# Kernel tuning notes

Hardware: AMD Instinct MI355X
Metric: run time of the kernel (lower is better)

The kernel has to match this reference:

```python
import jax, jax.numpy as jnp
import numpy as np

S_DIM = 128            # attention head width s
E_DIM = 1024           # expansion e = 2*hidden
SQRT_S = 128.0 ** 0.5
EPS = 1e-5


def setup_inputs() -> dict:
    key = jax.random.key(0)
    ks = jax.random.split(key, 8)
    B, S, H = 64, 512, 512
    uv_dim = 2 * E_DIM + S_DIM  # 2176
    # xavier-uniform-ish scale for uv weight
    lim = (6.0 / (H + uv_dim)) ** 0.5
    return {
        "x": jax.random.normal(ks[0], (B, S, H), dtype=jnp.float32),
        "ln_g": jnp.ones((1,), dtype=jnp.float32),
        "uv_w": jax.random.uniform(ks[1], (uv_dim, H), minval=-lim, maxval=lim, dtype=jnp.float32),
        "uv_b": jnp.zeros((uv_dim,), dtype=jnp.float32),
        "gamma": jax.random.uniform(ks[2], (2, S_DIM), dtype=jnp.float32),
        "beta": jax.random.uniform(ks[3], (2, S_DIM), dtype=jnp.float32),
        "w_bias": jax.random.uniform(ks[4], (2 * S - 1,), dtype=jnp.float32),
        "o_w": jax.random.normal(ks[5], (H, E_DIM), dtype=jnp.float32) * 0.02,
        "o_b": jnp.zeros((H,), dtype=jnp.float32),
    }


def _rope(x):
    # x: [B, S, 2, s]; rotate along the sequence dim (dim=1)
    S = x.shape[1]
    half = x.shape[-1] // 2
    pos = jnp.arange(S, dtype=jnp.float32)
    # torch: freq_seq = -arange(half)/half; inv_freq = 10000**(-freq_seq)
    inv_freq = 10000.0 ** (jnp.arange(half, dtype=jnp.float32) / half)
    sinus = pos[:, None, None] * inv_freq[None, None, :]  # [S, 1, half]
    sin, cos = jnp.sin(sinus), jnp.cos(sinus)
    x1, x2 = x[..., :half], x[..., half:]
    return jnp.concatenate([x1 * cos - x2 * sin, x2 * cos + x1 * sin], axis=-1)


def reference(x, ln_g, uv_w, uv_b, gamma, beta, w_bias, o_w, o_b):
    B, S, H = x.shape
    # ScaleNorm
    norm = jnp.linalg.norm(x, axis=-1, keepdims=True) * (H ** -0.5)
    xn = x / jnp.maximum(norm, EPS) * ln_g
    # fused uv projection + SiLU
    act = jax.nn.silu(xn @ uv_w.T + uv_b)  # [B, S, 2e+s]
    u = act[..., :E_DIM]
    v = act[..., E_DIM:2 * E_DIM]
    base = act[..., 2 * E_DIM:]                      # [B, S, s]
    base = base[:, :, None, :] * gamma + beta        # [B, S, 2, s]
    base = _rope(base)
    q, k = base[:, :, 0, :], base[:, :, 1, :]
    # scores + relative position bias: bias[i, j] = w[j - i + S - 1]
    qk = jnp.einsum('bsd,btd->bst', q, k)
    idx = jnp.arange(S)[None, :] - jnp.arange(S)[:, None] + (S - 1)
    qk = qk + w_bias[idx]
    # relu2 similarity kernel
    kernel = jnp.square(jax.nn.relu(qk / SQRT_S))    # [B, S, S]
    out = u * jnp.einsum('bst,bte->bse', kernel, v)  # gated attention
    out = out @ o_w.T + o_b
    return out + x  # use_shortcut: hidden == output
```

## Files before the change

### kernel.cpp

```cpp
#include <hip/hip_runtime.h>
#include <math.h>


#define M_TOT   32768
#define S_LEN   512
#define H_DIM   512
#define E_DIMC  1024
#define UV_DIM  2176
#define UV_PAD  2304
#define D_DIM   128

using floatx4  = __attribute__((ext_vector_type(4))) float;
using uintx2   = __attribute__((ext_vector_type(2))) unsigned int;
using uintx4   = __attribute__((ext_vector_type(4))) unsigned int;
using ushortx4 = __attribute__((ext_vector_type(4))) unsigned short;
using short8   = __attribute__((ext_vector_type(8))) short;

#define ASYNC_CP16(gsrc, ldst)                                                  \
    __builtin_amdgcn_global_load_lds(                                           \
        (const __attribute__((address_space(1))) void*)(gsrc),                  \
        (__attribute__((address_space(3))) void*)(ldst), 16, 0, 0)

__device__ __forceinline__ float bf2f(unsigned short h) {
    union { unsigned int u; float f; } c;
    c.u = ((unsigned int)h) << 16;
    return c.f;
}
__device__ __forceinline__ unsigned short f2bf(float f) {
    union { float f; unsigned int u; } c;
    c.f = f;
    unsigned int r = c.u + 0x7fffu + ((c.u >> 16) & 1u);
    return (unsigned short)(r >> 16);
}
__device__ __forceinline__ float silu_fast(float x) {
    float e = __expf(-x);
    return x * __builtin_amdgcn_rcpf(1.0f + e);
}
__device__ __forceinline__ int xcd_remap(int b, int nwg) {
    return (b & 7) * (nwg >> 3) + (b >> 3);
}

__global__ __launch_bounds__(256) void prep_kernel(const float* __restrict__ x,
                                                   const float* __restrict__ ln_g,
                                                   unsigned short* __restrict__ xn,
                                                   const float* __restrict__ uv_w,
                                                   unsigned short* __restrict__ uvwb,
                                                   const float* __restrict__ o_w,
                                                   unsigned short* __restrict__ owb,
                                                   float* __restrict__ cost,
                                                   float* __restrict__ sint) {
    const int bid = blockIdx.x;
    const int tid = threadIdx.x;
    if (bid < 8192) {
        int row  = bid * 4 + (tid >> 6);
        int lane = tid & 63;
        const float* xr = x + (size_t)row * H_DIM;
        floatx4 v0 = ((const floatx4*)xr)[lane];
        floatx4 v1 = ((const floatx4*)xr)[lane + 64];
        float ss = v0.x*v0.x + v0.y*v0.y + v0.z*v0.z + v0.w*v0.w
                 + v1.x*v1.x + v1.y*v1.y + v1.z*v1.z + v1.w*v1.w;
        #pragma unroll
        for (int off = 32; off > 0; off >>= 1) ss += __shfl_xor(ss, off, 64);
        float norm = sqrtf(ss) * 0.044194173824159216f;
        float sc   = ln_g[0] / fmaxf(norm, 1e-5f);
        unsigned short* xo = xn + (size_t)row * H_DIM;
        ushortx4 o0, o1;
        o0.x = f2bf(v0.x * sc); o0.y = f2bf(v0.y * sc);
        o0.z = f2bf(v0.z * sc); o0.w = f2bf(v0.w * sc);
        o1.x = f2bf(v1.x * sc); o1.y = f2bf(v1.y * sc);
        o1.z = f2bf(v1.z * sc); o1.w = f2bf(v1.w * sc);
        ((ushortx4*)xo)[lane]      = o0;
        ((ushortx4*)xo)[lane + 64] = o1;
    } else if (bid < 9344) {
        int i = (bid - 8192) * 256 + tid;
        ushortx4 o;
        if (i < UV_DIM * H_DIM / 4) {
            floatx4 v = ((const floatx4*)uv_w)[i];
            o.x = f2bf(v.x); o.y = f2bf(v.y); o.z = f2bf(v.z); o.w = f2bf(v.w);
        } else {
            o.x = 0; o.y = 0; o.z = 0; o.w = 0;
        }
        ((ushortx4*)uvwb)[i] = o;
    } else if (bid < 9856) {
        int i = (bid - 9344) * 256 + tid;
        floatx4 v = ((const floatx4*)o_w)[i];
        ushortx4 o;
        o.x = f2bf(v.x); o.y = f2bf(v.y); o.z = f2bf(v.z); o.w = f2bf(v.w);
        ((ushortx4*)owb)[i] = o;
    } else {
        int idx = (bid - 9856) * 256 + tid;
        int s = idx >> 6;
        int j = idx & 63;
        float invf = (float)pow(10000.0, (double)j / 64.0);
        float ang  = (float)s * invf;
        double a   = (double)ang;
        cost[s * 64 + j] = (float)cos(a);
        sint[s * 64 + j] = (float)sin(a);
    }
}

template <bool SWAPT>
__device__ __forceinline__ void gemm128_core(const unsigned short* __restrict__ A,
                                             const unsigned short* __restrict__ B,
                                             int lda, int ldb, int K,
                                             int m0, int n0,
                                             unsigned short (&st)[3][12288],
                                             floatx4 (&acc)[4][4]) {
    const int tid  = threadIdx.x;
    const int lane = tid & 63;
    const int wave = tid >> 6;
    const int quad = lane >> 4;
    const int l16  = lane & 15;
    const int wrow = (wave >> 2) * 64;
    const int wcol = (wave & 3) * 64;

    const int qa  = wave * 64 + lane;
    const int Ra  = qa >> 3;
    const int ca  = (qa & 7) ^ (Ra & 7);
    const int srA = 2 * Ra + (ca >> 2);
    const int scA = (ca & 3) * 8;
    const unsigned short* pa  = A + (size_t)(m0 + srA) * lda + scA;
    const unsigned short* pb0 = B + (size_t)(n0 + srA) * ldb + scA;
    const unsigned short* pb1 = pb0 + (size_t)128 * ldb;
    const int ldsA  = (wave * 64) * 8;
    const int ldsB0 = 4096 + (wave * 64) * 8;
    const int ldsB1 = 4096 + (512 + wave * 64) * 8;

    #pragma unroll
    for (int i = 0; i < 4; i++)
        #pragma unroll
        for (int j = 0; j < 4; j++) acc[i][j] = (floatx4){0.f, 0.f, 0.f, 0.f};

    const int NT = K >> 5;
    auto stage = [&](int buf, int t) {
        unsigned short* s = &st[buf][0];
        const int kt = t * 32;
        ASYNC_CP16(pa  + kt, s + ldsA);
        ASYNC_CP16(pb0 + kt, s + ldsB0);
        ASYNC_CP16(pb1 + kt, s + ldsB1);
    };
    stage(0, 0);
    stage(1, 1);

    int aoff[4], boff[4];
    #pragma unroll
    for (int mt = 0; mt < 4; mt++) {
        int r  = wrow + mt * 16 + l16;
        int Rr = r >> 1;
        int cp = (((r & 1) << 2) + quad) ^ (Rr & 7);
        aoff[mt] = Rr * 64 + cp * 8;
    }
    #pragma unroll
    for (int nt = 0; nt < 4; nt++) {
        int r  = wcol + nt * 16 + l16;
        int Rr = r >> 1;
        int cp = (((r & 1) << 2) + quad) ^ (Rr & 7);
        boff[nt] = 4096 + Rr * 64 + cp * 8;
    }

    int bc = 0, bs = 2;
    for (int t = 0; t < NT; ++t) {
        if (t < NT - 1) asm volatile("s_waitcnt vmcnt(3)" ::: "memory");
        else            asm volatile("s_waitcnt vmcnt(0)" ::: "memory");
        __builtin_amdgcn_sched_barrier(0);
        __builtin_amdgcn_s_barrier();
        __builtin_amdgcn_sched_barrier(0);
        if (t + 2 < NT) stage(bs, t + 2);

        const unsigned short* sb = &st[bc][0];
        short8 af[4], bf[4];
        #pragma unroll
        for (int mt = 0; mt < 4; mt++) {
            union { short8 s8; uintx4 u4; } fu;
            fu.u4 = *(const uintx4*)&sb[aoff[mt]];
            af[mt] = fu.s8;
        }
        #pragma unroll
        for (int nt = 0; nt < 4; nt++) {
            union { short8 s8; uintx4 u4; } fu;
            fu.u4 = *(const uintx4*)&sb[boff[nt]];
            bf[nt] = fu.s8;
        }
        __builtin_amdgcn_s_setprio(1);
        #pragma unroll
        for (int mt = 0; mt < 4; mt++)
            #pragma unroll
            for (int nt = 0; nt < 4; nt++)
                acc[mt][nt] = SWAPT
                    ? __builtin_amdgcn_mfma_f32_16x16x32_bf16(bf[nt], af[mt], acc[mt][nt], 0, 0, 0)
                    : __builtin_amdgcn_mfma_f32_16x16x32_bf16(af[mt], bf[nt], acc[mt][nt], 0, 0, 0);
        __builtin_amdgcn_s_setprio(0);

        bc = (bc == 2) ? 0 : bc + 1;
        bs = (bs == 2) ? 0 : bs + 1;
    }
}

union __align__(16) Lds3 {
    unsigned short st[3][12288];
    unsigned short T[128 * 256];
    float          Tf[128][132];
};

__global__ __launch_bounds__(512, 2) void gemm1_128_kernel(const unsigned short* __restrict__ xn,
                                                           const unsigned short* __restrict__ uvw,
                                                           const float* __restrict__ uvb,
                                                           unsigned short* __restrict__ u,
                                                           unsigned short* __restrict__ vT,
                                                           const float* __restrict__ gamma,
                                                           const float* __restrict__ beta,
                                                           const float* __restrict__ cost,
                                                           const float* __restrict__ sint,
                                                           unsigned short* __restrict__ q,
                                                           unsigned short* __restrict__ k) {
    __shared__ Lds3 lds;
    floatx4 acc[4][4];
    const int bl = blockIdx.y * 9 + blockIdx.x;
    const int lg = xcd_remap(bl, 9 * (M_TOT / 128));
    const int xb = lg % 9;
    const int m0 = (lg / 9) * 128;
    const int tid = threadIdx.x, lane = tid & 63, wave = tid >> 6;
    const int quad = lane >> 4, l16 = lane & 15;
    const int wrow = (wave >> 2) * 64, wcol = (wave & 3) * 64;

    if (xb < 4) {
        const int n0 = xb * 256;
        gemm128_core<true>(xn, uvw, H_DIM, H_DIM, H_DIM, m0, n0, lds.st, acc);
        __syncthreads();
        #pragma unroll
        for (int mt = 0; mt < 4; mt++) {
            int row = wrow + mt * 16 + l16;
            #pragma unroll
            for (int nt = 0; nt < 4; nt++) {
                int nl = wcol + nt * 16 + quad * 4;
                floatx4 b4 = *(const floatx4*)&uvb[n0 + nl];
                ushortx4 pk;
                #pragma unroll
                for (int r = 0; r < 4; r++)
                    pk[r] = f2bf(silu_fast(acc[mt][nt][r] + b4[r]));
                *(uintx2*)&lds.T[row * 256 + (((nl >> 3) ^ (row & 15)) << 3) + (nl & 7)] = *(uintx2*)&pk;
            }
        }
        __syncthreads();
        #pragma unroll
        for (int i = 0; i < 8; i++) {
            int idx = tid + i * 512;
            int row = idx >> 5, c16 = idx & 31;
            *(uintx4*)(u + (size_t)(m0 + row) * E_DIMC + n0 + c16 * 8) =
                *(const uintx4*)&lds.T[row * 256 + ((c16 ^ (row & 15)) << 3)];
        }
    } else if (xb < 8) {
        const int n0 = xb * 256;
        gemm128_core<false>(xn, uvw, H_DIM, H_DIM, H_DIM, m0, n0, lds.st, acc);
        __syncthreads();
        #pragma unroll
        for (int nt = 0; nt < 4; nt++) {
            int rowT = wcol + nt * 16 + l16;
            float bias = uvb[n0 + rowT];
            #pragma unroll
            for (int mt = 0; mt < 4; mt++) {
                int colT = wrow + mt * 16 + quad * 4;
                ushortx4 pk;
                #pragma unroll
                for (int r = 0; r < 4; r++)
                    pk[r] = f2bf(silu_fast(acc[mt][nt][r] + bias));
                *(uintx2*)&lds.T[rowT * 128 + (((colT >> 3) ^ (rowT & 15)) << 3) + (colT & 7)] = *(uintx2*)&pk;
            }
        }
        __syncthreads();
        const int b = m0 >> 9, sg0 = m0 & (S_LEN - 1), eg0 = n0 - E_DIMC;
        #pragma unroll
        for (int i = 0; i < 8; i++) {
            int idx = tid + i * 512;
            int e = idx >> 4, j = idx & 15;
            *(uintx4*)(vT + ((size_t)b * E_DIMC + eg0 + e) * S_LEN + sg0 + j * 8) =
                *(const uintx4*)&lds.T[e * 128 + ((j ^ (e & 15)) << 3)];
        }
    } else {
        const int n0 = 2048;
        gemm128_core<false>(xn, uvw, H_DIM, H_DIM, H_DIM, m0, n0, lds.st, acc);
        __syncthreads();
        if ((wave & 3) < 2) {
            #pragma unroll
            for (int mt = 0; mt < 4; mt++) {
                int rowl = wrow + mt * 16 + quad * 4;
                #pragma unroll
                for (int nt = 0; nt < 4; nt++) {
                    int n = wcol + nt * 16 + l16;
                    float bias = uvb[2048 + n];
                    #pragma unroll
                    for (int r = 0; r < 4; r++)
                        lds.Tf[rowl + r][n] = silu_fast(acc[mt][nt][r] + bias);
                }
            }
        }
        __syncthreads();
        #pragma unroll
        for (int i = 0; i < 16; i++) {
            int idx = tid + i * 512;
            int row = idx >> 6, j = idx & 63;
            int s   = (m0 + row) & (S_LEN - 1);
            float b1 = lds.Tf[row][j];
            float b2 = lds.Tf[row][j + 64];
            float c  = cost[s * 64 + j];
            float sn = sint[s * 64 + j];
            float yq1 = b1 * gamma[j]       + beta[j];
            float yq2 = b2 * gamma[64 + j]  + beta[64 + j];
            float yk1 = b1 * gamma[128 + j] + beta[128 + j];
            float yk2 = b2 * gamma[192 + j] + beta[192 + j];
            size_t mo = (size_t)(m0 + row) * D_DIM;
            q[mo + j]      = f2bf(yq1 * c - yq2 * sn);
            q[mo + 64 + j] = f2bf(yq2 * c + yq1 * sn);
            k[mo + j]      = f2bf(yk1 * c - yk2 * sn);
            k[mo + 64 + j] = f2bf(yk2 * c + yk1 * sn);
        }
    }
}

template <bool SWAPT>
__device__ __forceinline__ void gemm256_core(const unsigned short* __restrict__ A,
                                             const unsigned short* __restrict__ B,
                                             int lda, int ldb, int K,
                                             int m0, int n0,
                                             unsigned short (&st)[4][2][128][64],
                                             floatx4 (&acc)[8][4]) {
    const int tid  = threadIdx.x;
    const int lane = tid & 63;
    const int wave = tid >> 6;
    const int quad = lane >> 4;
    const int l16  = lane & 15;
    const int wrow = (wave >> 2) * 128;
    const int wcol = (wave & 3) * 64;

    const int q0    = wave * 128 + lane;
    const int R0    = q0 >> 3;
    const int cp0   = q0 & 7;
    const int c0    = cp0 ^ (R0 & 7);
    const int srow0 = 2 * R0 + (c0 >> 2);
    const int scol0 = (c0 & 3) * 8;

    const unsigned short* pa0 = A + (size_t)(m0 + srow0) * lda + scol0;
    const unsigned short* pa1 = pa0 + (size_t)16 * lda;
    const unsigned short* pb0 = B + (size_t)(n0 + srow0) * ldb + scol0;
    const unsigned short* pb1 = pb0 + (size_t)16 * ldb;
    const int ldsOff0 = (wave * 128) * 8;
    const int ldsOff1 = (wave * 128 + 64) * 8;

    #pragma unroll
    for (int i = 0; i < 8; i++)
        #pragma unroll
        for (int j = 0; j < 4; j++) acc[i][j] = (floatx4){0.f, 0.f, 0.f, 0.f};

    const int NT = K >> 5;
    auto stage = [&](int t) {
        unsigned short* sA = &st[t & 3][0][0][0];
        unsigned short* sB = &st[t & 3][1][0][0];
        const int kt = t * 32;
        ASYNC_CP16(pa0 + kt, sA + ldsOff0);
        ASYNC_CP16(pa1 + kt, sA + ldsOff1);
        ASYNC_CP16(pb0 + kt, sB + ldsOff0);
        ASYNC_CP16(pb1 + kt, sB + ldsOff1);
    };
    stage(0);
    stage(1);
    stage(2);

    int aoff[8], boff[4];
    #pragma unroll
    for (int mt = 0; mt < 8; mt++) {
        int r  = wrow + mt * 16 + l16;
        int Rr = r >> 1;
        int cp = (((r & 1) << 2) + quad) ^ (Rr & 7);
        aoff[mt] = Rr * 64 + cp * 8;
    }
    #pragma unroll
    for (int nt = 0; nt < 4; nt++) {
        int r  = wcol + nt * 16 + l16;
        int Rr = r >> 1;
        int cp = (((r & 1) << 2) + quad) ^ (Rr & 7);
        boff[nt] = Rr * 64 + cp * 8;
    }

    for (int t = 0; t < NT; ++t) {
        if (t < NT - 2)       asm volatile("s_waitcnt vmcnt(8)" ::: "memory");
        else if (t == NT - 2) asm volatile("s_waitcnt vmcnt(4)" ::: "memory");
        else                  asm volatile("s_waitcnt vmcnt(0)" ::: "memory");
        __builtin_amdgcn_sched_barrier(0);
        __builtin_amdgcn_s_barrier();
        __builtin_amdgcn_sched_barrier(0);
        if (t + 3 < NT) stage(t + 3);

        const unsigned short* sA = &st[t & 3][0][0][0];
        const unsigned short* sB = &st[t & 3][1][0][0];
        short8 bf[4];
        #pragma unroll
        for (int nt = 0; nt < 4; nt++) {
            union { short8 s8; uintx4 u4; } fu;
            fu.u4 = *(const uintx4*)&sB[boff[nt]];
            bf[nt] = fu.s8;
        }
        #pragma unroll
        for (int half = 0; half < 2; half++) {
            short8 af[4];
            #pragma unroll
            for (int mt = 0; mt < 4; mt++) {
                union { short8 s8; uintx4 u4; } fu;
                fu.u4 = *(const uintx4*)&sA[aoff[half * 4 + mt]];
                af[mt] = fu.s8;
            }
            __builtin_amdgcn_s_setprio(1);
            #pragma unroll
            for (int mt = 0; mt < 4; mt++)
                #pragma unroll
                for (int nt = 0; nt < 4; nt++)
                    acc[half * 4 + mt][nt] = SWAPT
                        ? __builtin_amdgcn_mfma_f32_16x16x32_bf16(bf[nt], af[mt], acc[half * 4 + mt][nt], 0, 0, 0)
                        : __builtin_amdgcn_mfma_f32_16x16x32_bf16(af[mt], bf[nt], acc[half * 4 + mt][nt], 0, 0, 0);
            __builtin_amdgcn_s_setprio(0);
        }
    }
}

__global__ __launch_bounds__(512, 2) void gemm_out256_kernel(const unsigned short* __restrict__ oe,
                                                             const unsigned short* __restrict__ ow,
                                                             const float* __restrict__ ob,
                                                             const float* __restrict__ x,
                                                             float* __restrict__ out) {
    __shared__ __align__(16) unsigned short st[4][2][128][64];
    floatx4 acc[8][4];
    const int bl = blockIdx.y * 2 + blockIdx.x;
    const int lg = xcd_remap(bl, 2 * (M_TOT / 256));
    const int n0 = (lg & 1) * 256;
    const int m0 = (lg >> 1) * 256;
    gemm256_core<true>(oe, ow, E_DIMC, E_DIMC, E_DIMC, m0, n0, st, acc);

    const int tid = threadIdx.x, lane = tid & 63, wave = tid >> 6;
    const int quad = lane >> 4, l16 = lane & 15;
    const int wrow = (wave >> 2) * 128, wcol = (wave & 3) * 64;
    #pragma unroll
    for (int mt = 0; mt < 8; mt++) {
        int m = m0 + wrow + mt * 16 + l16;
        #pragma unroll
        for (int nt = 0; nt < 4; nt++) {
            int n = n0 + wcol + nt * 16 + quad * 4;
            size_t off = (size_t)m * H_DIM + n;
            floatx4 b4 = *(const floatx4*)&ob[n];
            floatx4 x4 = *(const floatx4*)&x[off];
            *(floatx4*)&out[off] = acc[mt][nt] + b4 + x4;
        }
    }
}

struct GemmLds {
    unsigned short As[128 * 64];
    unsigned short Bs[128 * 64];
};

template <bool SWAPT>
__device__ __forceinline__ void gemm_bt_core(const unsigned short* __restrict__ A,
                                             const unsigned short* __restrict__ B,
                                             int lda, int ldb, int K,
                                             int m0, int n0,
                                             GemmLds& lds, floatx4 (&acc)[4][4]) {
    const int tid  = threadIdx.x;
    const int lane = tid & 63;
    const int wave = tid >> 6;
    const int quad = lane >> 4;
    const int l16  = lane & 15;
    const int wm   = (wave >> 1) * 64;
    const int wn   = (wave & 1) * 64;
    const int lrow = lane >> 3;
    const int cgs  = ((lane & 7) ^ lrow) * 8;

    #pragma unroll
    for (int i = 0; i < 4; i++)
        #pragma unroll
        for (int j = 0; j < 4; j++) acc[i][j] = (floatx4){0.f, 0.f, 0.f, 0.f};

    for (int kt = 0; kt < K; kt += 64) {
        #pragma unroll
        for (int i = 0; i < 4; i++) {
            int r0 = wave * 32 + i * 8;
            const unsigned short* ga = A + (size_t)(m0 + r0 + lrow) * lda + kt + cgs;
            const unsigned short* gb = B + (size_t)(n0 + r0 + lrow) * ldb + kt + cgs;
            ASYNC_CP16(ga, &lds.As[r0 * 64]);
            ASYNC_CP16(gb, &lds.Bs[r0 * 64]);
        }
        __syncthreads();
        #pragma unroll
        for (int kk = 0; kk < 64; kk += 32) {
            short8 af[4], bf[4];
            const int pc = (kk + quad * 8) ^ ((l16 & 7) * 8);
            #pragma unroll
            for (int mt = 0; mt < 4; mt++) {
                int row = wm + mt * 16 + l16;
                union { short8 s8; uintx4 u4; } fu;
                fu.u4 = *(const uintx4*)&lds.As[row * 64 + pc];
                af[mt] = fu.s8;
            }
            #pragma unroll
            for (int nt = 0; nt < 4; nt++) {
                int row = wn + nt * 16 + l16;
                union { short8 s8; uintx4 u4; } fu;
                fu.u4 = *(const uintx4*)&lds.Bs[row * 64 + pc];
                bf[nt] = fu.s8;
            }
            #pragma unroll
            for (int mt = 0; mt < 4; mt++)
                #pragma unroll
                for (int nt = 0; nt < 4; nt++)
                    acc[mt][nt] = SWAPT
                        ? __builtin_amdgcn_mfma_f32_16x16x32_bf16(bf[nt], af[mt], acc[mt][nt], 0, 0, 0)
                        : __builtin_amdgcn_mfma_f32_16x16x32_bf16(af[mt], bf[nt], acc[mt][nt], 0, 0, 0);
        }
        __syncthreads();
    }
}

union LdsU {
    GemmLds g;
    unsigned short T[128 * 128];
};
__device__ __forceinline__ int swz(int row, int col) {
    return row * 128 + ((((col >> 3) ^ (row & 7)) << 3) | (col & 7));
}

__global__ __launch_bounds__(256) void gemm_qk_kernel(const unsigned short* __restrict__ q,
                                                      const unsigned short* __restrict__ k,
                                                      const float* __restrict__ wbias,
                                                      unsigned short* __restrict__ P) {
    __shared__ LdsU lds;
    floatx4 acc[4][4];
    const int bl = (blockIdx.z * 4 + blockIdx.y) * 4 + blockIdx.x;
    const int lg = xcd_remap(bl, 1024);
    const int bx = lg & 3, by = (lg >> 2) & 3, bz = lg >> 4;
    size_t boff = (size_t)bz * S_LEN * D_DIM;
    unsigned short* Pb = P + (size_t)bz * S_LEN * S_LEN;
    const int m0 = bx * 128, n0 = by * 128;
    gemm_bt_core<true>(q + boff, k + boff, D_DIM, D_DIM, D_DIM, m0, n0, lds.g, acc);

    const int tid = threadIdx.x, lane = tid & 63, wave = tid >> 6;
    const int quad = lane >> 4, l16 = lane & 15;
    const int wm = (wave >> 1) * 64, wn = (wave & 1) * 64;
    #pragma unroll
    for (int mt = 0; mt < 4; mt++) {
        int row = wm + mt * 16 + l16;
        int s   = m0 + row;
        #pragma unroll
        for (int nt = 0; nt < 4; nt++) {
            int nl = wn + nt * 16 + quad * 4;
            int t0 = n0 + nl;
            ushortx4 pk;
            #pragma unroll
            for (int r = 0; r < 4; r++) {
                float z = (acc[mt][nt][r] + wbias[t0 + r - s + (S_LEN - 1)]) * 0.08838834764831845f;
                z = fmaxf(z, 0.f);
                pk[r] = f2bf(z * z);
            }
            *(uintx2*)&lds.T[swz(row, nl)] = *(uintx2*)&pk;
        }
    }
    __syncthreads();
    #pragma unroll
    for (int i = 0; i < 8; i++) {
        int idx = tid + i * 256;
        int row = idx >> 4;
        int j   = idx & 15;
        *(uintx4*)(Pb + (size_t)(m0 + row) * S_LEN + n0 + j * 8) =
            *(const uintx4*)&lds.T[swz(row, j * 8)];
    }
}

__global__ __launch_bounds__(256) void gemm_pv_kernel(const unsigned short* __restrict__ P,
                                                      const unsigned short* __restrict__ vT,
                                                      unsigned short* __restrict__ u) {
    __shared__ LdsU lds;
    floatx4 acc[4][4];
    const int bl = (blockIdx.z * 8 + blockIdx.y) * 4 + blockIdx.x;
    const int lg = xcd_remap(bl, 2048);
    const int bx = lg & 3, by = (lg >> 2) & 7, bb = lg >> 5;
    const unsigned short* Pb  = P  + (size_t)bb * S_LEN * S_LEN;
    const unsigned short* vTb = vT + (size_t)bb * E_DIMC * S_LEN;
    const int m0 = bx * 128, n0 = by * 128;
    gemm_bt_core<true>(Pb, vTb, S_LEN, S_LEN, S_LEN, m0, n0, lds.g, acc);

    const int tid = threadIdx.x, lane = tid & 63, wave = tid >> 6;
    const int quad = lane >> 4, l16 = lane & 15;
    const int wm = (wave >> 1) * 64, wn = (wave & 1) * 64;
    #pragma unroll
    for (int mt = 0; mt < 4; mt++) {
        int row = wm + mt * 16 + l16;
        #pragma unroll
        for (int nt = 0; nt < 4; nt++) {
            int nl = wn + nt * 16 + quad * 4;
            ushortx4 pk;
            #pragma unroll
            for (int r = 0; r < 4; r++) pk[r] = f2bf(acc[mt][nt][r]);
            *(uintx2*)&lds.T[swz(row, nl)] = *(uintx2*)&pk;
        }
    }
    __syncthreads();
    #pragma unroll
    for (int i = 0; i < 8; i++) {
        int idx = tid + i * 256;
        int row = idx >> 4;
        int j   = idx & 15;
        size_t off = ((size_t)bb * S_LEN + m0 + row) * E_DIMC + n0 + j * 8;
        union { uintx4 u4; unsigned short s[8]; } tv, uv, ov;
        tv.u4 = *(const uintx4*)&lds.T[swz(row, j * 8)];
        uv.u4 = *(const uintx4*)(u + off);
        #pragma unroll
        for (int jj = 0; jj < 8; jj++) ov.s[jj] = f2bf(bf2f(tv.s[jj]) * bf2f(uv.s[jj]));
        *(uintx4*)(u + off) = ov.u4;
    }
}

extern "C" void kernel_launch(void* const* d_in, const int* in_sizes, int n_in,
                              void* d_out, int out_size, void* d_ws, size_t ws_size,
                              hipStream_t stream) {
    const float* x     = (const float*)d_in[0];
    const float* ln_g  = (const float*)d_in[1];
    const float* uv_w  = (const float*)d_in[2];
    const float* uv_b  = (const float*)d_in[3];
    const float* gamma = (const float*)d_in[4];
    const float* beta  = (const float*)d_in[5];
    const float* wbias = (const float*)d_in[6];
    const float* o_w   = (const float*)d_in[7];
    const float* o_b   = (const float*)d_in[8];
    float* out = (float*)d_out;

    char* ws = (char*)d_ws;
    size_t off = 0;
    auto alloc = [&](size_t bytes) {
        void* p = ws + off;
        off += (bytes + 255) & ~(size_t)255;
        return p;
    };
    unsigned short* u     = (unsigned short*)alloc((size_t)M_TOT * E_DIMC * 2);
    unsigned short* vT    = (unsigned short*)alloc((size_t)64 * E_DIMC * S_LEN * 2);
    unsigned short* xn    = (unsigned short*)alloc((size_t)M_TOT * H_DIM * 2);
    unsigned short* P     = xn;
    unsigned short* q     = (unsigned short*)alloc((size_t)M_TOT * D_DIM * 2);
    unsigned short* k     = (unsigned short*)alloc((size_t)M_TOT * D_DIM * 2);
    float*          cost  = (float*)alloc((size_t)S_LEN * 64 * 4);
    float*          sint  = (float*)alloc((size_t)S_LEN * 64 * 4);
    unsigned short* uvwb  = (unsigned short*)alloc((size_t)UV_PAD * H_DIM * 2);
    unsigned short* owb   = (unsigned short*)alloc((size_t)H_DIM * E_DIMC * 2);
    (void)ws_size; (void)in_sizes; (void)n_in; (void)out_size;

    prep_kernel<<<9984, 256, 0, stream>>>(x, ln_g, xn, uv_w, uvwb, o_w, owb, cost, sint);

    gemm1_128_kernel<<<dim3(9, M_TOT / 128), 512, 0, stream>>>(
        xn, uvwb, uv_b, u, vT, gamma, beta, cost, sint, q, k);

    gemm_qk_kernel<<<dim3(S_LEN / 128, S_LEN / 128, 64), 256, 0, stream>>>(q, k, wbias, P);

    gemm_pv_kernel<<<dim3(S_LEN / 128, E_DIMC / 128, 64), 256, 0, stream>>>(P, vT, u);

    gemm_out256_kernel<<<dim3(H_DIM / 256, M_TOT / 256), 512, 0, stream>>>(u, owb, o_b, x, out);
}
```

Before: 354.7 us.

## Move QK and PV attention GEMMs onto the larger pipelined 256-wide GEMM cores

Replaces the simple 128x128, 256-thread QK and PV kernels with 512-thread versions. These reuse the existing multi-stage gemm128_core/gemm256_core (QK becomes 128x256 tiles, PV 256x256 tiles). The larger tiles raise operand reuse and replace the unpipelined single-buffer loop with the deeper pipelined core. Epilogues are rewritten for a 256-wide swizzled LDS staging area. The cost is fewer blocks (512 per kernel), so there is less parallelism and possibly lower occupancy.

```diff
diff --git a/kernel.cpp b/kernel.cpp
--- a/kernel.cpp
+++ b/kernel.cpp
@@ -421,6 +421,11 @@
     }
 }
 
+union __align__(16) Lds256 {
+    unsigned short st[4][2][128][64];
+    unsigned short T[256 * 256];
+};
+
 __global__ __launch_bounds__(512, 2) void gemm_out256_kernel(const unsigned short* __restrict__ oe,
                                                              const unsigned short* __restrict__ ow,
                                                              const float* __restrict__ ob,
@@ -451,104 +456,75 @@
     }
 }
 
-struct GemmLds {
-    unsigned short As[128 * 64];
-    unsigned short Bs[128 * 64];
-};
-
-template <bool SWAPT>
-__device__ __forceinline__ void gemm_bt_core(const unsigned short* __restrict__ A,
-                                             const unsigned short* __restrict__ B,
-                                             int lda, int ldb, int K,
-                                             int m0, int n0,
-                                             GemmLds& lds, floatx4 (&acc)[4][4]) {
-    const int tid  = threadIdx.x;
-    const int lane = tid & 63;
-    const int wave = tid >> 6;
-    const int quad = lane >> 4;
-    const int l16  = lane & 15;
-    const int wm   = (wave >> 1) * 64;
-    const int wn   = (wave & 1) * 64;
-    const int lrow = lane >> 3;
-    const int cgs  = ((lane & 7) ^ lrow) * 8;
-
-    #pragma unroll
-    for (int i = 0; i < 4; i++)
-        #pragma unroll
-        for (int j = 0; j < 4; j++) acc[i][j] = (floatx4){0.f, 0.f, 0.f, 0.f};
-
-    for (int kt = 0; kt < K; kt += 64) {
-        #pragma unroll
-        for (int i = 0; i < 4; i++) {
-            int r0 = wave * 32 + i * 8;
-            const unsigned short* ga = A + (size_t)(m0 + r0 + lrow) * lda + kt + cgs;
-            const unsigned short* gb = B + (size_t)(n0 + r0 + lrow) * ldb + kt + cgs;
-            ASYNC_CP16(ga, &lds.As[r0 * 64]);
-            ASYNC_CP16(gb, &lds.Bs[r0 * 64]);
-        }
-        __syncthreads();
-        #pragma unroll
-        for (int kk = 0; kk < 64; kk += 32) {
-            short8 af[4], bf[4];
-            const int pc = (kk + quad * 8) ^ ((l16 & 7) * 8);
-            #pragma unroll
-            for (int mt = 0; mt < 4; mt++) {
-                int row = wm + mt * 16 + l16;
-                union { short8 s8; uintx4 u4; } fu;
-                fu.u4 = *(const uintx4*)&lds.As[row * 64 + pc];
-                af[mt] = fu.s8;
-            }
-            #pragma unroll
-            for (int nt = 0; nt < 4; nt++) {
-                int row = wn + nt * 16 + l16;
-                union { short8 s8; uintx4 u4; } fu;
-                fu.u4 = *(const uintx4*)&lds.Bs[row * 64 + pc];
-                bf[nt] = fu.s8;
-            }
-            #pragma unroll
-            for (int mt = 0; mt < 4; mt++)
-                #pragma unroll
-                for (int nt = 0; nt < 4; nt++)
-                    acc[mt][nt] = SWAPT
-                        ? __builtin_amdgcn_mfma_f32_16x16x32_bf16(bf[nt], af[mt], acc[mt][nt], 0, 0, 0)
-                        : __builtin_amdgcn_mfma_f32_16x16x32_bf16(af[mt], bf[nt], acc[mt][nt], 0, 0, 0);
-        }
-        __syncthreads();
-    }
-}
-
-union LdsU {
-    GemmLds g;
-    unsigned short T[128 * 128];
-};
-__device__ __forceinline__ int swz(int row, int col) {
-    return row * 128 + ((((col >> 3) ^ (row & 7)) << 3) | (col & 7));
-}
-
-__global__ __launch_bounds__(256) void gemm_qk_kernel(const unsigned short* __restrict__ q,
-                                                      const unsigned short* __restrict__ k,
-                                                      const float* __restrict__ wbias,
-                                                      unsigned short* __restrict__ P) {
-    __shared__ LdsU lds;
+__global__ __launch_bounds__(512, 2) void gemm_pv256_kernel(const unsigned short* __restrict__ P,
+                                                            const unsigned short* __restrict__ vT,
+                                                            unsigned short* __restrict__ u) {
+    __shared__ Lds256 lds;
+    floatx4 acc[8][4];
+    const int bl = (blockIdx.z * 4 + blockIdx.y) * 2 + blockIdx.x;
+    const int lg = xcd_remap(bl, 512);
+    const int bx = lg & 1, by = (lg >> 1) & 3, bb = lg >> 3;
+    const unsigned short* Pb  = P  + (size_t)bb * S_LEN * S_LEN;
+    const unsigned short* vTb = vT + (size_t)bb * E_DIMC * S_LEN;
+    const int m0 = bx * 256, n0 = by * 256;
+    gemm256_core<true>(Pb, vTb, S_LEN, S_LEN, S_LEN, m0, n0, lds.st, acc);
+
+    const int tid = threadIdx.x, lane = tid & 63, wave = tid >> 6;
+    const int quad = lane >> 4, l16 = lane & 15;
+    const int wrow = (wave >> 2) * 128, wcol = (wave & 3) * 64;
+    __syncthreads();
+    #pragma unroll
+    for (int mt = 0; mt < 8; mt++) {
+        int row = wrow + mt * 16 + l16;
+        #pragma unroll
+        for (int nt = 0; nt < 4; nt++) {
+            int nl = wcol + nt * 16 + quad * 4;
+            ushortx4 pk;
+            #pragma unroll
+            for (int r = 0; r < 4; r++) pk[r] = f2bf(acc[mt][nt][r]);
+            *(uintx2*)&lds.T[row * 256 + (((nl >> 3) ^ (row & 15)) & 31) * 8 + (nl & 7)] = *(uintx2*)&pk;
+        }
+    }
+    __syncthreads();
+    #pragma unroll
+    for (int i = 0; i < 16; i++) {
+        int idx = tid + i * 512;
+        int row = idx >> 5, c16 = idx & 31;
+        size_t off = ((size_t)bb * S_LEN + m0 + row) * E_DIMC + n0 + c16 * 8;
+        union { uintx4 u4; unsigned short s[8]; } tv, uv, ov;
+        tv.u4 = *(const uintx4*)&lds.T[row * 256 + ((c16 ^ (row & 15)) * 8)];
+        uv.u4 = *(const uintx4*)(u + off);
+        #pragma unroll
+        for (int jj = 0; jj < 8; jj++) ov.s[jj] = f2bf(bf2f(tv.s[jj]) * bf2f(uv.s[jj]));
+        *(uintx4*)(u + off) = ov.u4;
+    }
+}
+
+__global__ __launch_bounds__(512, 2) void gemm_qk128_kernel(const unsigned short* __restrict__ q,
+                                                            const unsigned short* __restrict__ k,
+                                                            const float* __restrict__ wbias,
+                                                            unsigned short* __restrict__ P) {
+    __shared__ Lds3 lds;
     floatx4 acc[4][4];
-    const int bl = (blockIdx.z * 4 + blockIdx.y) * 4 + blockIdx.x;
-    const int lg = xcd_remap(bl, 1024);
-    const int bx = lg & 3, by = (lg >> 2) & 3, bz = lg >> 4;
+    const int bl = (blockIdx.z * 2 + blockIdx.y) * 4 + blockIdx.x;
+    const int lg = xcd_remap(bl, 512);
+    const int bx = lg & 3, by = (lg >> 2) & 1, bz = lg >> 3;
     size_t boff = (size_t)bz * S_LEN * D_DIM;
     unsigned short* Pb = P + (size_t)bz * S_LEN * S_LEN;
-    const int m0 = bx * 128, n0 = by * 128;
-    gemm_bt_core<true>(q + boff, k + boff, D_DIM, D_DIM, D_DIM, m0, n0, lds.g, acc);
+    const int m0 = bx * 128, n0 = by * 256;
+    gemm128_core<true>(q + boff, k + boff, D_DIM, D_DIM, D_DIM, m0, n0, lds.st, acc);
 
     const int tid = threadIdx.x, lane = tid & 63, wave = tid >> 6;
     const int quad = lane >> 4, l16 = lane & 15;
-    const int wm = (wave >> 1) * 64, wn = (wave & 1) * 64;
+    const int wrow = (wave >> 2) * 64, wcol = (wave & 3) * 64;
+    __syncthreads();
     #pragma unroll
     for (int mt = 0; mt < 4; mt++) {
-        int row = wm + mt * 16 + l16;
+        int row = wrow + mt * 16 + l16;
         int s   = m0 + row;
         #pragma unroll
         for (int nt = 0; nt < 4; nt++) {
-            int nl = wn + nt * 16 + quad * 4;
+            int nl = wcol + nt * 16 + quad * 4;
             int t0 = n0 + nl;
             ushortx4 pk;
             #pragma unroll
@@ -557,61 +533,16 @@
                 z = fmaxf(z, 0.f);
                 pk[r] = f2bf(z * z);
             }
-            *(uintx2*)&lds.T[swz(row, nl)] = *(uintx2*)&pk;
+            *(uintx2*)&lds.T[row * 256 + (((nl >> 3) ^ (row & 15)) << 3) + (nl & 7)] = *(uintx2*)&pk;
         }
     }
     __syncthreads();
     #pragma unroll
     for (int i = 0; i < 8; i++) {
-        int idx = tid + i * 256;
-        int row = idx >> 4;
-        int j   = idx & 15;
-        *(uintx4*)(Pb + (size_t)(m0 + row) * S_LEN + n0 + j * 8) =
-            *(const uintx4*)&lds.T[swz(row, j * 8)];
-    }
-}
-
-__global__ __launch_bounds__(256) void gemm_pv_kernel(const unsigned short* __restrict__ P,
-                                                      const unsigned short* __restrict__ vT,
-                                                      unsigned short* __restrict__ u) {
-    __shared__ LdsU lds;
-    floatx4 acc[4][4];
-    const int bl = (blockIdx.z * 8 + blockIdx.y) * 4 + blockIdx.x;
-    const int lg = xcd_remap(bl, 2048);
-    const int bx = lg & 3, by = (lg >> 2) & 7, bb = lg >> 5;
-    const unsigned short* Pb  = P  + (size_t)bb * S_LEN * S_LEN;
-    const unsigned short* vTb = vT + (size_t)bb * E_DIMC * S_LEN;
-    const int m0 = bx * 128, n0 = by * 128;
-    gemm_bt_core<true>(Pb, vTb, S_LEN, S_LEN, S_LEN, m0, n0, lds.g, acc);
-
-    const int tid = threadIdx.x, lane = tid & 63, wave = tid >> 6;
-    const int quad = lane >> 4, l16 = lane & 15;
-    const int wm = (wave >> 1) * 64, wn = (wave & 1) * 64;
-    #pragma unroll
-    for (int mt = 0; mt < 4; mt++) {
-        int row = wm + mt * 16 + l16;
-        #pragma unroll
-        for (int nt = 0; nt < 4; nt++) {
-            int nl = wn + nt * 16 + quad * 4;
-            ushortx4 pk;
-            #pragma unroll
-            for (int r = 0; r < 4; r++) pk[r] = f2bf(acc[mt][nt][r]);
-            *(uintx2*)&lds.T[swz(row, nl)] = *(uintx2*)&pk;
-        }
-    }
-    __syncthreads();
-    #pragma unroll
-    for (int i = 0; i < 8; i++) {
-        int idx = tid + i * 256;
-        int row = idx >> 4;
-        int j   = idx & 15;
-        size_t off = ((size_t)bb * S_LEN + m0 + row) * E_DIMC + n0 + j * 8;
-        union { uintx4 u4; unsigned short s[8]; } tv, uv, ov;
-        tv.u4 = *(const uintx4*)&lds.T[swz(row, j * 8)];
-        uv.u4 = *(const uintx4*)(u + off);
-        #pragma unroll
-        for (int jj = 0; jj < 8; jj++) ov.s[jj] = f2bf(bf2f(tv.s[jj]) * bf2f(uv.s[jj]));
-        *(uintx4*)(u + off) = ov.u4;
+        int idx = tid + i * 512;
+        int row = idx >> 5, c16 = idx & 31;
+        *(uintx4*)(Pb + (size_t)(m0 + row) * S_LEN + n0 + c16 * 8) =
+            *(const uintx4*)&lds.T[row * 256 + ((c16 ^ (row & 15)) << 3)];
     }
 }
 
@@ -653,9 +584,9 @@
     gemm1_128_kernel<<<dim3(9, M_TOT / 128), 512, 0, stream>>>(
         xn, uvwb, uv_b, u, vT, gamma, beta, cost, sint, q, k);
 
-    gemm_qk_kernel<<<dim3(S_LEN / 128, S_LEN / 128, 64), 256, 0, stream>>>(q, k, wbias, P);
-
-    gemm_pv_kernel<<<dim3(S_LEN / 128, E_DIMC / 128, 64), 256, 0, stream>>>(P, vT, u);
+    gemm_qk128_kernel<<<dim3(4, 2, 64), 512, 0, stream>>>(q, k, wbias, P);
+
+    gemm_pv256_kernel<<<dim3(2, 4, 64), 512, 0, stream>>>(P, vT, u);
 
     gemm_out256_kernel<<<dim3(H_DIM / 256, M_TOT / 256), 512, 0, stream>>>(u, owb, o_b, x, out);
 }
```

After: 358.5 us, median of 2. No clear change (+1.1%).
